# Kernel tuning notes

Hardware: AMD Instinct MI355X
Metric: run time of the kernel (lower is better)

Reference implementation:

```python
import jax, jax.numpy as jnp
import numpy as np

W_MAX = 256  # max words per sentence (word ids 1..W_MAX; 0 = special/pad subwords)


def setup_inputs() -> dict:
    key = jax.random.key(0)
    k1, k2 = jax.random.split(key)
    L, B, S, F = 4, 32, 512, 768
    hidden_states = jax.random.normal(k1, (L, B, S, F), dtype=jnp.float32)
    layer_weights = jnp.ones((L,), dtype=jnp.float32)
    gamma = jnp.ones((1,), dtype=jnp.float32)
    # contiguous ragged word spans: sorted word ids per subword position
    word_ids = jnp.sort(
        jax.random.randint(k2, (B, S), 0, W_MAX + 1, dtype=jnp.int32), axis=1
    )
    return {
        "hidden_states": hidden_states,
        "layer_weights": layer_weights,
        "gamma": gamma,
        "word_ids": word_ids,
    }


def reference(hidden_states, layer_weights, gamma, word_ids):
    L, B, S, F = hidden_states.shape
    num_seg = B * (W_MAX + 1)

    # weighted layer mixing (weight_layers=True branch)
    normal_weights = jax.nn.softmax(layer_weights)
    subword_embeddings = gamma * jnp.einsum("l,lbsf->bsf", normal_weights, hidden_states)

    # fused segment-mean over ragged word spans
    flat = subword_embeddings.reshape(B * S, F)
    seg = (word_ids + jnp.arange(B, dtype=word_ids.dtype)[:, None] * (W_MAX + 1)).reshape(-1)
    sums = jax.ops.segment_sum(flat, seg, num_segments=num_seg)
    counts = jax.ops.segment_sum(
        jnp.ones((B * S,), dtype=flat.dtype), seg, num_segments=num_seg
    )
    means = sums / jnp.maximum(counts, 1.0)[:, None]  # empty words stay zero

    word_embeddings = means.reshape(B, W_MAX + 1, F)
    # slot 0: mean over all subword positions (sentence embedding)
    word_embeddings = word_embeddings.at[:, 0, :].set(subword_embeddings.mean(axis=1))
    return word_embeddings
```

## Files before the change

### kernel.cpp

```cpp
#include <hip/hip_runtime.h>

#define LL 4
#define BB 32
#define SS 512
#define FF 768
#define NW 257
#define F4 192

__device__ __forceinline__ void f4add(float4& a, const float4& b) {
    a.x += b.x; a.y += b.y; a.z += b.z; a.w += b.w;
}

__global__ void k_counts(const int* __restrict__ wid, int* __restrict__ counts) {
    __shared__ int lc[NW];
    int b = blockIdx.x;
    for (int i = threadIdx.x; i < NW; i += blockDim.x) lc[i] = 0;
    __syncthreads();
    atomicAdd(&lc[wid[b * SS + threadIdx.x]], 1);
    __syncthreads();
    for (int i = threadIdx.x; i < NW; i += blockDim.x) counts[b * NW + i] = lc[i];
}

__global__ void k_main(const float* __restrict__ hs, const float* __restrict__ lw,
                       const float* __restrict__ gm, const int* __restrict__ wid,
                       float* __restrict__ out, float* __restrict__ partials) {
    int bid = blockIdx.x;
    int fc = bid % 3;
    int sg = (bid / 3) & 7;
    int b  = bid / 24;
    int t = threadIdx.x;
    int lane = t & 63;
    int swave = t >> 6;
    int f4 = fc * 64 + lane;
    int s0 = sg * 64 + swave * 16;

    float w0 = lw[0], w1 = lw[1], w2 = lw[2], w3 = lw[3];
    float mx = fmaxf(fmaxf(w0, w1), fmaxf(w2, w3));
    float e0 = __expf(w0 - mx), e1 = __expf(w1 - mx);
    float e2 = __expf(w2 - mx), e3 = __expf(w3 - mx);
    float g = gm[0] / (e0 + e1 + e2 + e3);
    float c0 = e0 * g, c1 = e1 * g, c2 = e2 * g, c3 = e3 * g;

    const float4* h4 = (const float4*)hs;
    const int ls = BB * SS * F4;
    int base = (b * SS + s0) * F4 + f4;
    const int* wrow = wid + b * SS + s0;

    int prev = wrow[0];
    bool sharedL = (s0 > 0) && (wrow[-1] == prev);
    bool sharedR = (s0 + 16 < SS) && (wrow[16] == wrow[15]);

    float4 sent = {0.f, 0.f, 0.f, 0.f};
    float4 run  = {0.f, 0.f, 0.f, 0.f};
    bool first = true;

    #pragma unroll
    for (int k = 0; k < 16; k++) {
        int w = wrow[k];
        int idx = base + k * F4;
        float4 a  = h4[idx];
        float4 bv = h4[idx + ls];
        float4 cv = h4[idx + 2 * ls];
        float4 dv = h4[idx + 3 * ls];
        float4 v;
        v.x = c0 * a.x + c1 * bv.x + c2 * cv.x + c3 * dv.x;
        v.y = c0 * a.y + c1 * bv.y + c2 * cv.y + c3 * dv.y;
        v.z = c0 * a.z + c1 * bv.z + c2 * cv.z + c3 * dv.z;
        v.w = c0 * a.w + c1 * bv.w + c2 * cv.w + c3 * dv.w;
        f4add(sent, v);
        if (w != prev) {
            float* p = out + (prev + b * NW) * FF + f4 * 4;
            if (first && sharedL) {
                atomicAdd(p + 0, run.x); atomicAdd(p + 1, run.y);
                atomicAdd(p + 2, run.z); atomicAdd(p + 3, run.w);
            } else {
                *(float4*)p = run;
            }
            first = false;
            run = v; prev = w;
        } else {
            f4add(run, v);
        }
    }
    {
        float* p = out + (prev + b * NW) * FF + f4 * 4;
        if ((first && sharedL) || sharedR) {
            atomicAdd(p + 0, run.x); atomicAdd(p + 1, run.y);
            atomicAdd(p + 2, run.z); atomicAdd(p + 3, run.w);
        } else {
            *(float4*)p = run;
        }
    }

    __shared__ float4 sm[256];
    sm[t] = sent;
    __syncthreads();
    if (t < 64) {
        float4 tot = sm[t];
        f4add(tot, sm[t + 64]);
        f4add(tot, sm[t + 128]);
        f4add(tot, sm[t + 192]);
        ((float4*)partials)[(b * 8 + sg) * F4 + f4] = tot;
    }
}

__global__ void k_means(float* __restrict__ out, const int* __restrict__ counts) {
    int t = blockIdx.x * 256 + threadIdx.x;
    if (t >= BB * NW * F4) return;
    int f4 = t % F4;
    int r = t / F4;
    int w = r % NW;
    int b = r / NW;
    if (w == 0) return;
    int c = counts[b * NW + w];
    float inv = 1.0f / (float)(c > 1 ? c : 1);
    float4* p = (float4*)out + (b * NW + w) * F4 + f4;
    float4 v = *p;
    v.x *= inv; v.y *= inv; v.z *= inv; v.w *= inv;
    *p = v;
}

__global__ void k_sent(const float* __restrict__ partials, float* __restrict__ out) {
    int t = blockIdx.x * 256 + threadIdx.x;
    if (t >= BB * F4) return;
    int f4 = t % F4;
    int b = t / F4;
    const float4* p4 = (const float4*)partials;
    float4 tot = {0.f, 0.f, 0.f, 0.f};
    #pragma unroll
    for (int g = 0; g < 8; g++) f4add(tot, p4[(b * 8 + g) * F4 + f4]);
    const float s = 1.0f / (float)SS;
    tot.x *= s; tot.y *= s; tot.z *= s; tot.w *= s;
    ((float4*)out)[(size_t)b * NW * F4 + f4] = tot;
}

extern "C" void kernel_launch(void* const* d_in, const int* in_sizes, int n_in,
                              void* d_out, int out_size, void* d_ws, size_t ws_size,
                              hipStream_t stream) {
    const float* hs  = (const float*)d_in[0];
    const float* lw  = (const float*)d_in[1];
    const float* gm  = (const float*)d_in[2];
    const int*   wid = (const int*)d_in[3];
    float* out = (float*)d_out;

    int*   counts   = (int*)d_ws;
    float* partials = (float*)((char*)d_ws + 33024);

    hipMemsetAsync(d_out, 0, (size_t)out_size * sizeof(float), stream);
    k_counts<<<BB, 512, 0, stream>>>(wid, counts);
    k_main<<<BB * 24, 256, 0, stream>>>(hs, lw, gm, wid, out, partials);
    int nm = BB * NW * F4;
    k_means<<<(nm + 255) / 256, 256, 0, stream>>>(out, counts);
    k_sent<<<(BB * F4 + 255) / 256, 256, 0, stream>>>(partials, out);
}
```

Baseline: 305.1 us.

## Fold mean division into main kernel, merge counts/means/sentence into one fix kernel

Words that lie entirely within one 16-row chunk are now divided by their local length inside the main kernel. Only words spanning chunk boundaries get a later rescale in a single per-sentence fixup kernel, which also computes counts and the sentence-mean slot. This drops the separate counts kernel and the full-output read-modify-write means pass. The change also switches to nontemporal loads and sets launch bounds, but the fixup kernel loops serially over all word ids per block.

```diff
diff --git a/kernel.cpp b/kernel.cpp
--- a/kernel.cpp
+++ b/kernel.cpp
@@ -7,23 +7,12 @@
 #define NW 257
 #define F4 192
 
-__device__ __forceinline__ void f4add(float4& a, const float4& b) {
-    a.x += b.x; a.y += b.y; a.z += b.z; a.w += b.w;
-}
+typedef float f4v __attribute__((ext_vector_type(4)));
 
-__global__ void k_counts(const int* __restrict__ wid, int* __restrict__ counts) {
-    __shared__ int lc[NW];
-    int b = blockIdx.x;
-    for (int i = threadIdx.x; i < NW; i += blockDim.x) lc[i] = 0;
-    __syncthreads();
-    atomicAdd(&lc[wid[b * SS + threadIdx.x]], 1);
-    __syncthreads();
-    for (int i = threadIdx.x; i < NW; i += blockDim.x) counts[b * NW + i] = lc[i];
-}
-
-__global__ void k_main(const float* __restrict__ hs, const float* __restrict__ lw,
-                       const float* __restrict__ gm, const int* __restrict__ wid,
-                       float* __restrict__ out, float* __restrict__ partials) {
+__global__ __launch_bounds__(256, 3)
+void k_main(const float* __restrict__ hs, const float* __restrict__ lw,
+            const float* __restrict__ gm, const int* __restrict__ wid,
+            float* __restrict__ out, float* __restrict__ partials) {
     int bid = blockIdx.x;
     int fc = bid % 3;
     int sg = (bid / 3) & 7;
@@ -41,7 +30,7 @@
     float g = gm[0] / (e0 + e1 + e2 + e3);
     float c0 = e0 * g, c1 = e1 * g, c2 = e2 * g, c3 = e3 * g;
 
-    const float4* h4 = (const float4*)hs;
+    const f4v* h4 = (const f4v*)hs;
     const int ls = BB * SS * F4;
     int base = (b * SS + s0) * F4 + f4;
     const int* wrow = wid + b * SS + s0;
@@ -50,36 +39,33 @@
     bool sharedL = (s0 > 0) && (wrow[-1] == prev);
     bool sharedR = (s0 + 16 < SS) && (wrow[16] == wrow[15]);
 
-    float4 sent = {0.f, 0.f, 0.f, 0.f};
-    float4 run  = {0.f, 0.f, 0.f, 0.f};
+    f4v sent = {0.f, 0.f, 0.f, 0.f};
+    f4v run  = {0.f, 0.f, 0.f, 0.f};
+    int len = 0;
     bool first = true;
 
     #pragma unroll
     for (int k = 0; k < 16; k++) {
         int w = wrow[k];
         int idx = base + k * F4;
-        float4 a  = h4[idx];
-        float4 bv = h4[idx + ls];
-        float4 cv = h4[idx + 2 * ls];
-        float4 dv = h4[idx + 3 * ls];
-        float4 v;
-        v.x = c0 * a.x + c1 * bv.x + c2 * cv.x + c3 * dv.x;
-        v.y = c0 * a.y + c1 * bv.y + c2 * cv.y + c3 * dv.y;
-        v.z = c0 * a.z + c1 * bv.z + c2 * cv.z + c3 * dv.z;
-        v.w = c0 * a.w + c1 * bv.w + c2 * cv.w + c3 * dv.w;
-        f4add(sent, v);
+        f4v a  = __builtin_nontemporal_load(&h4[idx]);
+        f4v bv = __builtin_nontemporal_load(&h4[idx + ls]);
+        f4v cv = __builtin_nontemporal_load(&h4[idx + 2 * ls]);
+        f4v dv = __builtin_nontemporal_load(&h4[idx + 3 * ls]);
+        f4v v = c0 * a + c1 * bv + c2 * cv + c3 * dv;
+        sent += v;
         if (w != prev) {
             float* p = out + (prev + b * NW) * FF + f4 * 4;
             if (first && sharedL) {
                 atomicAdd(p + 0, run.x); atomicAdd(p + 1, run.y);
                 atomicAdd(p + 2, run.z); atomicAdd(p + 3, run.w);
             } else {
-                *(float4*)p = run;
+                *(f4v*)p = run * (1.0f / (float)len);
             }
             first = false;
-            run = v; prev = w;
+            run = v; len = 1; prev = w;
         } else {
-            f4add(run, v);
+            run += v; len++;
         }
     }
     {
@@ -88,50 +74,48 @@
             atomicAdd(p + 0, run.x); atomicAdd(p + 1, run.y);
             atomicAdd(p + 2, run.z); atomicAdd(p + 3, run.w);
         } else {
-            *(float4*)p = run;
+            *(f4v*)p = run * (1.0f / (float)len);
         }
     }
 
-    __shared__ float4 sm[256];
+    __shared__ f4v sm[256];
     sm[t] = sent;
     __syncthreads();
     if (t < 64) {
-        float4 tot = sm[t];
-        f4add(tot, sm[t + 64]);
-        f4add(tot, sm[t + 128]);
-        f4add(tot, sm[t + 192]);
-        ((float4*)partials)[(b * 8 + sg) * F4 + f4] = tot;
+        f4v tot = sm[t] + sm[t + 64] + sm[t + 128] + sm[t + 192];
+        ((f4v*)partials)[(b * 8 + sg) * F4 + f4] = tot;
     }
 }
 
-__global__ void k_means(float* __restrict__ out, const int* __restrict__ counts) {
-    int t = blockIdx.x * 256 + threadIdx.x;
-    if (t >= BB * NW * F4) return;
-    int f4 = t % F4;
-    int r = t / F4;
-    int w = r % NW;
-    int b = r / NW;
-    if (w == 0) return;
-    int c = counts[b * NW + w];
-    float inv = 1.0f / (float)(c > 1 ? c : 1);
-    float4* p = (float4*)out + (b * NW + w) * F4 + f4;
-    float4 v = *p;
-    v.x *= inv; v.y *= inv; v.z *= inv; v.w *= inv;
-    *p = v;
-}
-
-__global__ void k_sent(const float* __restrict__ partials, float* __restrict__ out) {
-    int t = blockIdx.x * 256 + threadIdx.x;
-    if (t >= BB * F4) return;
-    int f4 = t % F4;
-    int b = t / F4;
-    const float4* p4 = (const float4*)partials;
-    float4 tot = {0.f, 0.f, 0.f, 0.f};
-    #pragma unroll
-    for (int g = 0; g < 8; g++) f4add(tot, p4[(b * 8 + g) * F4 + f4]);
-    const float s = 1.0f / (float)SS;
-    tot.x *= s; tot.y *= s; tot.z *= s; tot.w *= s;
-    ((float4*)out)[(size_t)b * NW * F4 + f4] = tot;
+__global__ void k_fix(const int* __restrict__ wid,
+                      const float* __restrict__ partials,
+                      float* __restrict__ out) {
+    __shared__ int lc[NW];
+    __shared__ int flag[NW];
+    int b = blockIdx.x;
+    int t = threadIdx.x;
+    for (int i = t; i < NW; i += 512) { lc[i] = 0; flag[i] = 0; }
+    __syncthreads();
+    int w = wid[b * SS + t];
+    atomicAdd(&lc[w], 1);
+    if (t > 0 && (t & 15) == 0) {
+        if (wid[b * SS + t - 1] == w) flag[w] = 1;
+    }
+    __syncthreads();
+    for (int w2 = 1; w2 < NW; ++w2) {
+        if (flag[w2]) {
+            float inv = 1.0f / (float)(lc[w2] > 1 ? lc[w2] : 1);
+            float* p = out + ((size_t)b * NW + w2) * FF;
+            for (int f = t; f < FF; f += 512) p[f] *= inv;
+        }
+    }
+    const float* pp = partials + (size_t)b * 8 * FF;
+    for (int f = t; f < FF; f += 512) {
+        float s = 0.f;
+        #pragma unroll
+        for (int gg = 0; gg < 8; gg++) s += pp[gg * FF + f];
+        out[(size_t)b * NW * FF + f] = s * (1.0f / (float)SS);
+    }
 }
 
 extern "C" void kernel_launch(void* const* d_in, const int* in_sizes, int n_in,
@@ -143,13 +127,9 @@
     const int*   wid = (const int*)d_in[3];
     float* out = (float*)d_out;
 
-    int*   counts   = (int*)d_ws;
-    float* partials = (float*)((char*)d_ws + 33024);
+    float* partials = (float*)d_ws;
 
-    hipMemsetAsync(d_out, 0, (size_t)out_size * sizeof(float), stream);
-    k_counts<<<BB, 512, 0, stream>>>(wid, counts);
+    (void)hipMemsetAsync(d_out, 0, (size_t)out_size * sizeof(float), stream);
     k_main<<<BB * 24, 256, 0, stream>>>(hs, lw, gm, wid, out, partials);
-    int nm = BB * NW * F4;
-    k_means<<<(nm + 255) / 256, 256, 0, stream>>>(out, counts);
-    k_sent<<<(BB * F4 + 255) / 256, 256, 0, stream>>>(partials, out);
+    k_fix<<<BB, 512, 0, stream>>>(wid, partials, out);
 }
```

New measurement: 309.0 us. No clear change (+1.3%).
